# Performance work log

Hardware: AMD Instinct MI355X
Metric: run time of the kernel (lower is better)

## Reference

```python
import jax, jax.numpy as jnp
import numpy as np
from jax.scipy.special import logsumexp

NEG = -1e9  # grad-safe stand-in for -inf in the log-semiring chart
SMOOTH_RATIO = 0.9   # config.structure_smoothing_p


def _inside(lp, lengths):
    """CKY inside algorithm (TreeCRF partition).

    lp: [B, N, N, L] span log-potentials (lp[b, i, j, l] = span (i..j) with label l)
    Returns logZ per batch element: beta(0, len-1).
    Recursion: beta(i,j) = logsumexp_l lp[i,j,l] + logsumexp_{k=i..j-1} beta(i,k)+beta(k+1,j)
    Charts are kept in (start, width) and (end, width) layout so every width
    step is a fully vectorized roll + logsumexp over splits.
    """
    B, N = lp.shape[0], lp.shape[1]
    pot_node = logsumexp(lp, axis=-1)                       # [B, N, N]
    i = jnp.arange(N)
    j = (i[:, None] + i[None, :]) % N
    pot_span = pot_node[:, i[:, None], j]                   # [B, start, width]
    diag = pot_span[:, :, 0]                                # width-0 spans
    init = jnp.full((B, N, N), NEG, dtype=lp.dtype)
    cs = init.at[:, :, 0].set(diag)                         # cs[b,i,u] = beta(i, i+u)
    ce = cs                                                 # ce[b,j,u] = beta(j-u, j)
    u = jnp.arange(N)[None, None, :]
    starts = jnp.arange(N)[None, :]

    def step(carry, xs):
        cs, ce = carry
        w, pot_w = xs
        right = jnp.roll(ce, -w, axis=1)                    # right[b,i] = ce[b, i+w]
        # align so right_al[b,i,u] = ce[b, i+w, w-1-u] = beta(i+u+1, i+w)
        right_al = jnp.roll(right[:, :, ::-1], w - N, axis=2)
        comb = jnp.where(u < w, cs + right_al, NEG)         # splits k = i+u, u in [0,w)
        inner = logsumexp(comb, axis=2)                     # [B, N]
        newv = jnp.where(starts < N - w, inner + pot_w, NEG)
        cs = jax.lax.dynamic_update_slice_in_dim(cs, newv[:, :, None], w, axis=2)
        ce_new = jnp.roll(newv, w, axis=1)[:, :, None]      # reindex start -> end = start+w
        ce = jax.lax.dynamic_update_slice_in_dim(ce, ce_new, w, axis=2)
        return (cs, ce), None

    ws = jnp.arange(1, N)
    pots = jnp.moveaxis(pot_span, 2, 0)[1:]                 # [N-1, B, N]
    (cs, ce), _ = jax.lax.scan(step, (cs, ce), (ws, pots))
    return jnp.take_along_axis(cs[:, 0, :], (lengths - 1)[:, None], axis=1)[:, 0]


def setup_inputs() -> dict:
    key = jax.random.key(0)
    k1, k2, k3, k4 = jax.random.split(key, 4)
    B, N, L = 16, 256, 32
    log_potentials = jax.random.normal(k1, (B, N, N, L), dtype=jnp.float32)
    mask = (jax.random.uniform(k2, (B, N, N, L)) < 0.9).astype(jnp.float32)
    eval_mask = (jax.random.uniform(k3, (B, N, N, L)) < 0.9).astype(jnp.float32)
    lengths = jax.random.randint(k4, (B,), N // 2, N + 1)
    return {"log_potentials": log_potentials, "mask": mask,
            "lengths": lengths, "eval_mask": eval_mask}


def reference(log_potentials, mask, lengths, eval_mask):
    B = log_potentials.shape[0]
    # potential normalization (torch .std() is unbiased, ddof=1)
    flat = log_potentials.reshape(B, -1)
    mean = flat.mean(-1)
    var = ((flat - mean[:, None]) ** 2).sum(-1) / (flat.shape[1] - 1)
    std = jnp.sqrt(var)
    lp = (log_potentials - mean[:, None, None, None]) / std[:, None, None, None]

    z_full = _inside(lp, lengths)
    # CRF entropy: H = logZ - <marginals, theta>, marginals = d logZ / d theta
    marg = jax.grad(lambda p: _inside(p, lengths).sum())(lp)
    entropy = z_full - (marg * lp).sum((1, 2, 3))

    # structure smoothing (structure_smoothing_p = 0.9 < 1.0)
    mask_smooth = eval_mask + (1.0 - eval_mask) * (1.0 - SMOOTH_RATIO)
    z_smooth = _inside(lp + jnp.log(mask_smooth + 1e-10), lengths)
    log_prob_smooth = z_smooth - z_full

    # partially-masked partition
    z_partial = _inside(lp - 1e6 * (1.0 - eval_mask), lengths)
    log_prob = z_partial - z_full
    return (log_prob, log_prob_smooth, entropy)
```

## Files before the change

kernel.cpp:

```cpp
#include <hip/hip_runtime.h>
#include <math.h>

#define B_ 16
#define N_ 256
#define L_ 32
#define NN_ (N_*N_)
#define NNL_ (NN_*L_)
#define ANN_ (B_*NN_)
#define POTS_OFF 4096
#define NEGINF -1.0e30f
#define LOG2E_F 1.4426950408889634f
#define LN2_F   0.6931471805599453f

#if __has_builtin(__builtin_amdgcn_exp2f)
#define EX2(x) __builtin_amdgcn_exp2f(x)
#else
#define EX2(x) exp2f(x)
#endif
#if __has_builtin(__builtin_amdgcn_logf)
#define LG2(x) __builtin_amdgcn_logf(x)
#else
#define LG2(x) log2f(x)
#endif


__global__ void stats_partial(const float* __restrict__ lp, double* __restrict__ part) {
    int blk = blockIdx.x;
    int b = blk >> 5, seg = blk & 31;
    const float4* p4 = (const float4*)(lp + (size_t)b * NNL_ + (size_t)seg * (NNL_ / 32));
    double s = 0.0, ss = 0.0;
    for (int idx = threadIdx.x; idx < (NNL_ / 32 / 4); idx += 256) {
        float4 v = p4[idx];
        s  += (double)v.x + (double)v.y + (double)v.z + (double)v.w;
        ss += (double)v.x * v.x + (double)v.y * v.y + (double)v.z * v.z + (double)v.w * v.w;
    }
    __shared__ double sh0[256], sh1[256];
    sh0[threadIdx.x] = s; sh1[threadIdx.x] = ss;
    __syncthreads();
    for (int off = 128; off > 0; off >>= 1) {
        if (threadIdx.x < off) {
            sh0[threadIdx.x] += sh0[threadIdx.x + off];
            sh1[threadIdx.x] += sh1[threadIdx.x + off];
        }
        __syncthreads();
    }
    if (threadIdx.x == 0) { part[blk * 2] = sh0[0]; part[blk * 2 + 1] = sh1[0]; }
}

__global__ void stats_final(const double* __restrict__ part, float* __restrict__ stats) {
    int b = threadIdx.x;
    if (b >= B_) return;
    double s = 0.0, ss = 0.0;
    for (int k = 0; k < 32; ++k) { s += part[(b * 32 + k) * 2]; ss += part[(b * 32 + k) * 2 + 1]; }
    double n = (double)NNL_;
    double mean = s / n;
    double var = (ss - s * s / n) / (n - 1.0);
    stats[b * 2]     = (float)mean;
    stats[b * 2 + 1] = (float)(1.0 / sqrt(var));
}

__global__ __launch_bounds__(256)
void pots_kernel(const float* __restrict__ lp, const float* __restrict__ evm,
                 const float* __restrict__ stats, float* __restrict__ W) {
    int t = blockIdx.x * 256 + threadIdx.x;
    int b = t >> 16;
    int rem = t & (NN_ - 1);
    int i = rem >> 8;
    int w = rem & (N_ - 1);
    if (i + w >= N_) return;
    int j = i + w;
    const float4* xp = (const float4*)(lp  + ((size_t)(b * NN_ + i * N_ + j) << 5));
    const float4* ep = (const float4*)(evm + ((size_t)(b * NN_ + i * N_ + j) << 5));
    float mean = stats[b * 2], invstd = stats[b * 2 + 1];
    float m1 = NEGINF, s1 = 0.f, n1 = 0.f;
    float m2 = NEGINF, s2 = 0.f;
    float m3 = NEGINF, s3 = 0.f;
#pragma unroll
    for (int c = 0; c < 8; ++c) {
        float4 xv = xp[c];
        float4 em = ep[c];
        float x0 = (xv.x - mean) * invstd, x1 = (xv.y - mean) * invstd;
        float x2 = (xv.z - mean) * invstd, x3 = (xv.w - mean) * invstd;
        {
            float cm = fmaxf(fmaxf(x0, x1), fmaxf(x2, x3));
            float nm = fmaxf(m1, cm);
            float sc = __expf(m1 - nm);
            float e0 = __expf(x0 - nm), e1 = __expf(x1 - nm);
            float e2 = __expf(x2 - nm), e3 = __expf(x3 - nm);
            s1 = s1 * sc + (e0 + e1 + e2 + e3);
            n1 = n1 * sc + (e0 * x0 + e1 * x1 + e2 * x2 + e3 * x3);
            m1 = nm;
        }
        {
            float y0 = x0 + __logf(fmaf(em.x, 0.9f, 0.1f) + 1e-10f);
            float y1 = x1 + __logf(fmaf(em.y, 0.9f, 0.1f) + 1e-10f);
            float y2 = x2 + __logf(fmaf(em.z, 0.9f, 0.1f) + 1e-10f);
            float y3 = x3 + __logf(fmaf(em.w, 0.9f, 0.1f) + 1e-10f);
            float cm = fmaxf(fmaxf(y0, y1), fmaxf(y2, y3));
            float nm = fmaxf(m2, cm);
            float sc = __expf(m2 - nm);
            s2 = s2 * sc + __expf(y0 - nm) + __expf(y1 - nm) + __expf(y2 - nm) + __expf(y3 - nm);
            m2 = nm;
        }
        {
            float z0 = fmaf(em.x, 1e6f, x0 - 1e6f);
            float z1 = fmaf(em.y, 1e6f, x1 - 1e6f);
            float z2 = fmaf(em.z, 1e6f, x2 - 1e6f);
            float z3 = fmaf(em.w, 1e6f, x3 - 1e6f);
            float cm = fmaxf(fmaxf(z0, z1), fmaxf(z2, z3));
            float nm = fmaxf(m3, cm);
            float sc = __expf(m3 - nm);
            s3 = s3 * sc + __expf(z0 - nm) + __expf(z1 - nm) + __expf(z2 - nm) + __expf(z3 - nm);
            m3 = nm;
        }
    }
    int o = b * NN_ + i * N_ + w;
    W[POTS_OFF + 0 * ANN_ + o] = (m1 + __logf(s1)) * LOG2E_F;
    W[POTS_OFF + 1 * ANN_ + o] = n1 / s1;
    W[POTS_OFF + 2 * ANN_ + o] = (m2 + __logf(s2)) * LOG2E_F;
    W[POTS_OFF + 3 * ANN_ + o] = (m3 + __logf(s3)) * LOG2E_F;
}

__device__ __forceinline__ int lds_base(int i) {
    int a = i >> 5, c = i & 31;
    return ((8 * a - ((a * (a - 1)) >> 1)) << 10) + ((c * (8 - a)) << 5);
}
__device__ __forceinline__ int lds_addr(int i, int u) {
    return lds_base(i) + ((((u >> 2) ^ (i & 7)) << 2) | (u & 3));
}

__device__ __forceinline__ float4 ld4u(const float* p) {
    float4 v; __builtin_memcpy(&v, p, 16); return v;
}

template <bool EXPM, int LOGG>
__device__ __forceinline__ void stepw(
    float* __restrict__ SL,
    const float* __restrict__ pot, const float* __restrict__ sbr,
    float* __restrict__ EGe, float* __restrict__ EGh, float* __restrict__ SGh,
    const int w, const int cells, const int tid)
{
    constexpr int G = 1 << LOGG;
    const int group = tid >> LOGG;
    const int l = tid & (G - 1);
    if (group >= cells) return;
    const int i = group;
    const int j = i + w;
    const int ib = lds_base(i);
    const int isw = i & 7;
    const float* egE = EGe + j * N_;
    const int W4 = (w + 3) >> 2;
    float m = NEGINF, s = 0.f, n = 0.f;
    for (int mu = l; mu < W4; mu += G) {
        const int u0 = mu << 2;
        const float4 Lv = *(const float4*)&SL[ib + ((mu ^ isw) << 2)];
        const float4 Rv = ld4u(egE + (w - 4 - u0));
        float e0 = Lv.x + Rv.w;
        float e1 = Lv.y + Rv.z;
        float e2 = Lv.z + Rv.y;
        float e3 = Lv.w + Rv.x;
        const int rem = w - u0;
        if (rem < 4) {
            if (rem < 2) e1 = NEGINF;
            if (rem < 3) e2 = NEGINF;
            e3 = NEGINF;
        }
        float cm = fmaxf(fmaxf(e0, e1), fmaxf(e2, e3));
        float nm = fmaxf(m, cm);
        float sc = EX2(m - nm);
        float E0 = EX2(e0 - nm), E1 = EX2(e1 - nm);
        float E2 = EX2(e2 - nm), E3 = EX2(e3 - nm);
        s = s * sc + ((E0 + E1) + (E2 + E3));
        if constexpr (EXPM) {
            const float4 Hl = *(const float4*)(SGh + i * N_ + u0);
            const float4 Hr = ld4u(EGh + j * N_ + (w - 4 - u0));
            float h0 = Hl.x + Hr.w, h1 = Hl.y + Hr.z;
            float h2 = Hl.z + Hr.y, h3 = Hl.w + Hr.x;
            if (rem < 4) {
                if (rem < 2) h1 = 0.f;
                if (rem < 3) h2 = 0.f;
                h3 = 0.f;
            }
            n = n * sc + ((E0 * h0 + E1 * h1) + (E2 * h2 + E3 * h3));
        }
        m = nm;
    }
#pragma unroll
    for (int k = 1; k < G; k <<= 1) {
        float mo = __shfl_xor(m, k);
        float so = __shfl_xor(s, k);
        float no = 0.f;
        if constexpr (EXPM) no = __shfl_xor(n, k);
        float nm = fmaxf(m, mo);
        float a  = EX2(m - nm), bb = EX2(mo - nm);
        s = s * a + so * bb;
        if constexpr (EXPM) n = n * a + no * bb;
        m = nm;
    }
    if (l == 0) {
        float v = pot[i * N_ + w] + m + LG2(s);
        SL[lds_addr(i, w)] = v;
        EGe[j * N_ + w] = v;
        if constexpr (EXPM) {
            float hv = sbr[i * N_ + w] + n / s;
            SGh[i * N_ + w] = hv;
            EGh[j * N_ + w] = hv;
        }
    }
}

template <bool EXPM>
__device__ __forceinline__ void cky_loop(
    float* __restrict__ SL,
    const float* __restrict__ pot, const float* __restrict__ sbr,
    float* __restrict__ EGe, float* __restrict__ EGh, float* __restrict__ SGh,
    const int len, const int tid)
{
    for (int i = tid; i < len; i += 1024) {
        float v = pot[i * N_];
        SL[lds_addr(i, 0)] = v;
        EGe[i * N_] = v;
        if constexpr (EXPM) { float h0 = sbr[i * N_]; SGh[i * N_] = h0; EGh[i * N_] = h0; }
    }
    __syncthreads();
    for (int w = 1; w < len; ++w) {
        const int cells = len - w;
        if (cells > 128)      stepw<EXPM, 2>(SL, pot, sbr, EGe, EGh, SGh, w, cells, tid);
        else if (cells > 64)  stepw<EXPM, 3>(SL, pot, sbr, EGe, EGh, SGh, w, cells, tid);
        else if (cells > 32)  stepw<EXPM, 4>(SL, pot, sbr, EGe, EGh, SGh, w, cells, tid);
        else if (cells > 16)  stepw<EXPM, 5>(SL, pot, sbr, EGe, EGh, SGh, w, cells, tid);
        else                  stepw<EXPM, 6>(SL, pot, sbr, EGe, EGh, SGh, w, cells, tid);
        __syncthreads();
    }
}

__global__ __launch_bounds__(1024, 1)
void cky_all(float* __restrict__ W, const int* __restrict__ lengths) {
    __shared__ float SL[36864];
    const int bx = blockIdx.x;
    const int p = bx >> 4, b = bx & 15;
    const int tid = threadIdx.x;
    int len = lengths[b];
    if (len < 1) len = 1;
    if (len > N_) len = N_;
    float* zres = W + POTS_OFF + 9 * ANN_;

    if (p == 0) {
        const float* pot = W + POTS_OFF + 0 * ANN_ + b * NN_;
        const float* sbr = W + POTS_OFF + 1 * ANN_ + b * NN_;
        float* EGe = W + POTS_OFF + 4 * ANN_ + b * NN_;
        float* EGh = W + POTS_OFF + 5 * ANN_ + b * NN_;
        float* SGh = W + POTS_OFF + 6 * ANN_ + b * NN_;
        cky_loop<true>(SL, pot, sbr, EGe, EGh, SGh, len, tid);
        if (tid == 0) {
            zres[b]      = SL[lds_addr(0, len - 1)];
            zres[48 + b] = SGh[len - 1];
        }
    } else {
        const float* pot = W + POTS_OFF + (p == 1 ? 2 : 3) * ANN_ + b * NN_;
        float* EGe = W + POTS_OFF + (p == 1 ? 7 : 8) * ANN_ + b * NN_;
        cky_loop<false>(SL, pot, nullptr, EGe, nullptr, nullptr, len, tid);
        if (tid == 0) zres[p * 16 + b] = SL[lds_addr(0, len - 1)];
    }
}

__global__ void combine_kernel(const float* __restrict__ W, float* __restrict__ out) {
    int b = threadIdx.x;
    if (b >= B_) return;
    const float* zres = W + POTS_OFF + 9 * ANN_;
    float zf = zres[b], zs = zres[16 + b], zp = zres[32 + b], hr = zres[48 + b];
    out[b]          = (zp - zf) * LN2_F;
    out[16 + b]     = (zs - zf) * LN2_F;
    out[32 + b]     = zf * LN2_F - hr;
}

extern "C" void kernel_launch(void* const* d_in, const int* in_sizes, int n_in,
                              void* d_out, int out_size, void* d_ws, size_t ws_size,
                              hipStream_t stream) {
    const float* lp      = (const float*)d_in[0];
    const int*   lengths = (const int*)d_in[2];
    const float* evm     = (const float*)d_in[3];
    float*  W    = (float*)d_ws;
    double* part = (double*)d_ws;
    float*  stats = W + 2048;
    float*  out  = (float*)d_out;

    stats_partial<<<B_ * 32, 256, 0, stream>>>(lp, part);
    stats_final<<<1, 64, 0, stream>>>(part, stats);
    pots_kernel<<<(B_ * NN_) / 256, 256, 0, stream>>>(lp, evm, stats, W);
    cky_all<<<3 * B_, 1024, 0, stream>>>(W, lengths);
    combine_kernel<<<1, 64, 0, stream>>>(W, out);
}
```

Measured before the change: 907.7 us.

## Reverse end-chart layout, pack splits as float2, fold pots grid over triangle

The end-indexed charts (EGe/EGh) are now stored reversed, so the right operand lines up with the left operand and no per-element reversal is needed. The split loop is unrolled by two chunks with packed float2 arithmetic, and the ragged tail is handled once by a single lane instead of being masked on every iteration. The pots kernel folds the lower triangle onto the upper so half as many threads cover every valid span without idle threads. This adds code complexity and a tail path that must stay correct for every width.

```diff
diff --git a/kernel.cpp b/kernel.cpp
--- a/kernel.cpp
+++ b/kernel.cpp
@@ -12,6 +12,8 @@
 #define LOG2E_F 1.4426950408889634f
 #define LN2_F   0.6931471805599453f
 
+typedef float v2f __attribute__((ext_vector_type(2)));
+
 #if __has_builtin(__builtin_amdgcn_exp2f)
 #define EX2(x) __builtin_amdgcn_exp2f(x)
 #else
@@ -23,6 +25,10 @@
 #define LG2(x) log2f(x)
 #endif
 
+__device__ __forceinline__ v2f f4lo(float4 v) { v2f r; r.x = v.x; r.y = v.y; return r; }
+__device__ __forceinline__ v2f f4hi(float4 v) { v2f r; r.x = v.z; r.y = v.w; return r; }
+__device__ __forceinline__ v2f v2max(v2f a, v2f b) { return __builtin_elementwise_max(a, b); }
+
 
 __global__ void stats_partial(const float* __restrict__ lp, double* __restrict__ part) {
     int blk = blockIdx.x;
@@ -59,19 +65,13 @@
     stats[b * 2 + 1] = (float)(1.0 / sqrt(var));
 }
 
-__global__ __launch_bounds__(256)
-void pots_kernel(const float* __restrict__ lp, const float* __restrict__ evm,
-                 const float* __restrict__ stats, float* __restrict__ W) {
-    int t = blockIdx.x * 256 + threadIdx.x;
-    int b = t >> 16;
-    int rem = t & (NN_ - 1);
-    int i = rem >> 8;
-    int w = rem & (N_ - 1);
-    if (i + w >= N_) return;
+__device__ __forceinline__ void pots_cell(
+    const float* __restrict__ lp, const float* __restrict__ evm,
+    float mean, float invstd, int b, int i, int w, float* __restrict__ W)
+{
     int j = i + w;
     const float4* xp = (const float4*)(lp  + ((size_t)(b * NN_ + i * N_ + j) << 5));
     const float4* ep = (const float4*)(evm + ((size_t)(b * NN_ + i * N_ + j) << 5));
-    float mean = stats[b * 2], invstd = stats[b * 2 + 1];
     float m1 = NEGINF, s1 = 0.f, n1 = 0.f;
     float m2 = NEGINF, s2 = 0.f;
     float m3 = NEGINF, s3 = 0.f;
@@ -121,6 +121,21 @@
     W[POTS_OFF + 3 * ANN_ + o] = (m3 + __logf(s3)) * LOG2E_F;
 }
 
+__global__ __launch_bounds__(256)
+void pots_kernel(const float* __restrict__ lp, const float* __restrict__ evm,
+                 const float* __restrict__ stats, float* __restrict__ W) {
+    int t = blockIdx.x * 256 + threadIdx.x;
+    int b = t >> 15;
+    int rem = t & (NN_ / 2 - 1);
+    int i = rem >> 8;
+    int w = rem & (N_ - 1);
+    float mean = stats[b * 2], invstd = stats[b * 2 + 1];
+    int sum = i + w;
+    if (sum <= N_ - 1) pots_cell(lp, evm, mean, invstd, b, i, w, W);
+    else               pots_cell(lp, evm, mean, invstd, b, N_ - 1 - i, N_ - 1 - w, W);
+    if (sum == N_ - 1) pots_cell(lp, evm, mean, invstd, b, N_ - 1 - i, N_ - 1 - w, W);
+}
+
 __device__ __forceinline__ int lds_base(int i) {
     int a = i >> 5, c = i & 31;
     return ((8 * a - ((a * (a - 1)) >> 1)) << 10) + ((c * (8 - a)) << 5);
@@ -148,43 +163,110 @@
     const int j = i + w;
     const int ib = lds_base(i);
     const int isw = i & 7;
-    const float* egE = EGe + j * N_;
-    const int W4 = (w + 3) >> 2;
-    float m = NEGINF, s = 0.f, n = 0.f;
-    for (int mu = l; mu < W4; mu += G) {
+    const float* egE = EGe + j * N_ + (N_ - w);
+    const float* egH = nullptr;
+    const float* sgH = nullptr;
+    if constexpr (EXPM) { egH = EGh + j * N_ + (N_ - w); sgH = SGh + i * N_; }
+    const float pw = pot[i * N_ + w];
+    float sb = 0.f;
+    if constexpr (EXPM) sb = sbr[i * N_ + w];
+
+    const int F = w >> 2;
+    const int r = w & 3;
+
+    float m = NEGINF;
+    v2f s2; s2.x = 0.f; s2.y = 0.f;
+    v2f n2; n2.x = 0.f; n2.y = 0.f;
+
+    int mu = l;
+    for (; mu + G < F; mu += 2 * G) {
+        const int ua = mu << 2, ub = (mu + G) << 2;
+        const float4 La = *(const float4*)&SL[ib + ((mu ^ isw) << 2)];
+        const float4 Lb = *(const float4*)&SL[ib + (((mu + G) ^ isw) << 2)];
+        const float4 Ra = ld4u(egE + ua);
+        const float4 Rb = ld4u(egE + ub);
+        v2f ea0 = f4lo(La) + f4lo(Ra);
+        v2f ea1 = f4hi(La) + f4hi(Ra);
+        v2f eb0 = f4lo(Lb) + f4lo(Rb);
+        v2f eb1 = f4hi(Lb) + f4hi(Rb);
+        v2f mx = v2max(v2max(ea0, ea1), v2max(eb0, eb1));
+        float nm = fmaxf(m, fmaxf(mx.x, mx.y));
+        float sc = EX2(m - nm);
+        v2f nmv; nmv.x = nm; nmv.y = nm;
+        v2f scv; scv.x = sc; scv.y = sc;
+        v2f d0 = ea0 - nmv, d1 = ea1 - nmv, d2 = eb0 - nmv, d3 = eb1 - nmv;
+        v2f E0; E0.x = EX2(d0.x); E0.y = EX2(d0.y);
+        v2f E1; E1.x = EX2(d1.x); E1.y = EX2(d1.y);
+        v2f E2; E2.x = EX2(d2.x); E2.y = EX2(d2.y);
+        v2f E3; E3.x = EX2(d3.x); E3.y = EX2(d3.y);
+        s2 = s2 * scv + ((E0 + E1) + (E2 + E3));
+        if constexpr (EXPM) {
+            const float4 Ha = *(const float4*)(sgH + ua);
+            const float4 Hb = *(const float4*)(sgH + ub);
+            const float4 Qa = ld4u(egH + ua);
+            const float4 Qb = ld4u(egH + ub);
+            v2f ha0 = f4lo(Ha) + f4lo(Qa);
+            v2f ha1 = f4hi(Ha) + f4hi(Qa);
+            v2f hb0 = f4lo(Hb) + f4lo(Qb);
+            v2f hb1 = f4hi(Hb) + f4hi(Qb);
+            v2f t = E0 * ha0 + E1 * ha1;
+            v2f u = E2 * hb0 + E3 * hb1;
+            n2 = n2 * scv + (t + u);
+        }
+        m = nm;
+    }
+    if (mu < F) {
         const int u0 = mu << 2;
         const float4 Lv = *(const float4*)&SL[ib + ((mu ^ isw) << 2)];
-        const float4 Rv = ld4u(egE + (w - 4 - u0));
-        float e0 = Lv.x + Rv.w;
-        float e1 = Lv.y + Rv.z;
-        float e2 = Lv.z + Rv.y;
-        float e3 = Lv.w + Rv.x;
-        const int rem = w - u0;
-        if (rem < 4) {
-            if (rem < 2) e1 = NEGINF;
-            if (rem < 3) e2 = NEGINF;
-            e3 = NEGINF;
-        }
-        float cm = fmaxf(fmaxf(e0, e1), fmaxf(e2, e3));
-        float nm = fmaxf(m, cm);
+        const float4 Rv = ld4u(egE + u0);
+        v2f e0 = f4lo(Lv) + f4lo(Rv);
+        v2f e1 = f4hi(Lv) + f4hi(Rv);
+        v2f mx = v2max(e0, e1);
+        float nm = fmaxf(m, fmaxf(mx.x, mx.y));
         float sc = EX2(m - nm);
-        float E0 = EX2(e0 - nm), E1 = EX2(e1 - nm);
-        float E2 = EX2(e2 - nm), E3 = EX2(e3 - nm);
-        s = s * sc + ((E0 + E1) + (E2 + E3));
-        if constexpr (EXPM) {
-            const float4 Hl = *(const float4*)(SGh + i * N_ + u0);
-            const float4 Hr = ld4u(EGh + j * N_ + (w - 4 - u0));
-            float h0 = Hl.x + Hr.w, h1 = Hl.y + Hr.z;
-            float h2 = Hl.z + Hr.y, h3 = Hl.w + Hr.x;
-            if (rem < 4) {
-                if (rem < 2) h1 = 0.f;
-                if (rem < 3) h2 = 0.f;
-                h3 = 0.f;
-            }
-            n = n * sc + ((E0 * h0 + E1 * h1) + (E2 * h2 + E3 * h3));
+        v2f nmv; nmv.x = nm; nmv.y = nm;
+        v2f scv; scv.x = sc; scv.y = sc;
+        v2f d0 = e0 - nmv, d1 = e1 - nmv;
+        v2f E0; E0.x = EX2(d0.x); E0.y = EX2(d0.y);
+        v2f E1; E1.x = EX2(d1.x); E1.y = EX2(d1.y);
+        s2 = s2 * scv + (E0 + E1);
+        if constexpr (EXPM) {
+            const float4 Hl = *(const float4*)(sgH + u0);
+            const float4 Qv = ld4u(egH + u0);
+            v2f h0 = f4lo(Hl) + f4lo(Qv);
+            v2f h1 = f4hi(Hl) + f4hi(Qv);
+            n2 = n2 * scv + (E0 * h0 + E1 * h1);
         }
         m = nm;
     }
+    if (r && l == (F & (G - 1))) {
+        const int u0 = F << 2;
+        const float4 Lv = *(const float4*)&SL[ib + ((F ^ isw) << 2)];
+        const float4 Rv = ld4u(egE + u0);
+        float e0 = Lv.x + Rv.x;
+        float e1 = (r > 1) ? (Lv.y + Rv.y) : NEGINF;
+        float e2 = (r > 2) ? (Lv.z + Rv.z) : NEGINF;
+        float nm = fmaxf(m, fmaxf(fmaxf(e0, e1), e2));
+        float sc = EX2(m - nm);
+        float E0 = EX2(e0 - nm), E1 = EX2(e1 - nm), E2 = EX2(e2 - nm);
+        v2f scv; scv.x = sc; scv.y = sc;
+        v2f add; add.x = E0 + E2; add.y = E1;
+        s2 = s2 * scv + add;
+        if constexpr (EXPM) {
+            const float4 Hl = *(const float4*)(sgH + u0);
+            const float4 Qv = ld4u(egH + u0);
+            float h0 = Hl.x + Qv.x;
+            float h1 = (r > 1) ? (Hl.y + Qv.y) : 0.f;
+            float h2 = (r > 2) ? (Hl.z + Qv.z) : 0.f;
+            v2f na; na.x = E0 * h0 + E2 * h2; na.y = E1 * h1;
+            n2 = n2 * scv + na;
+        }
+        m = nm;
+    }
+
+    float s = s2.x + s2.y;
+    float n = 0.f;
+    if constexpr (EXPM) n = n2.x + n2.y;
 #pragma unroll
     for (int k = 1; k < G; k <<= 1) {
         float mo = __shfl_xor(m, k);
@@ -198,13 +280,13 @@
         m = nm;
     }
     if (l == 0) {
-        float v = pot[i * N_ + w] + m + LG2(s);
+        float v = pw + m + LG2(s);
         SL[lds_addr(i, w)] = v;
-        EGe[j * N_ + w] = v;
-        if constexpr (EXPM) {
-            float hv = sbr[i * N_ + w] + n / s;
+        EGe[j * N_ + (N_ - 1 - w)] = v;
+        if constexpr (EXPM) {
+            float hv = sb + n / s;
+            EGh[j * N_ + (N_ - 1 - w)] = hv;
             SGh[i * N_ + w] = hv;
-            EGh[j * N_ + w] = hv;
         }
     }
 }
@@ -219,8 +301,12 @@
     for (int i = tid; i < len; i += 1024) {
         float v = pot[i * N_];
         SL[lds_addr(i, 0)] = v;
-        EGe[i * N_] = v;
-        if constexpr (EXPM) { float h0 = sbr[i * N_]; SGh[i * N_] = h0; EGh[i * N_] = h0; }
+        EGe[i * N_ + (N_ - 1)] = v;
+        if constexpr (EXPM) {
+            float h0 = sbr[i * N_];
+            EGh[i * N_ + (N_ - 1)] = h0;
+            SGh[i * N_] = h0;
+        }
     }
     __syncthreads();
     for (int w = 1; w < len; ++w) {
@@ -287,7 +373,7 @@
 
     stats_partial<<<B_ * 32, 256, 0, stream>>>(lp, part);
     stats_final<<<1, 64, 0, stream>>>(part, stats);
-    pots_kernel<<<(B_ * NN_) / 256, 256, 0, stream>>>(lp, evm, stats, W);
+    pots_kernel<<<(B_ * NN_ / 2) / 256, 256, 0, stream>>>(lp, evm, stats, W);
     cky_all<<<3 * B_, 1024, 0, stream>>>(W, lengths);
     combine_kernel<<<1, 64, 0, stream>>>(W, out);
 }
```

After: 949.6 us. 1.05x slower.
